# Kernel tuning notes

Measured on AMD Instinct MI355X. Metric: run time of the kernel, lower is better.

The kernel has to match this reference:

```python
import jax, jax.numpy as jnp
import numpy as np
import math

V = 4096; E = 768; H = 12; NL = 4; FFN = 2048; B = 1; L = 2048; HD = E // H
EPS = 1e-5

def _alibi_slopes(n):
    def pow2(m):
        start = 2.0 ** (-2.0 ** (-(math.log2(m) - 3)))
        return [start * start ** i for i in range(m)]
    if math.log2(n).is_integer():
        return np.array(pow2(n), dtype=np.float32)
    c = 2 ** math.floor(math.log2(n))
    s = pow2(c) + pow2(2 * c)[0::2][: n - c]
    return np.array(s, dtype=np.float32)

def _alibi_bias():
    slopes = _alibi_slopes(H)                                   # (H,)
    pos = np.arange(L)
    rel = (pos[None, :] - pos[:, None]).astype(np.float32)      # (L,L), j - i
    return jnp.asarray(slopes[:, None, None] * rel[None])       # (H,L,L)

def _ln(x, g, b):
    m = x.mean(-1, keepdims=True)
    v = ((x - m) ** 2).mean(-1, keepdims=True)
    return (x - m) / jnp.sqrt(v + EPS) * g + b

def setup_inputs():
    key = jax.random.key(0)
    ks = jax.random.split(key, 10)
    s = 0.02
    def rn(k, shape):
        return jax.random.normal(k, shape, dtype=jnp.float32) * s
    embed = rn(ks[0], (V, E)).at[0].set(0.0)   # padding_idx=0 row zeroed
    return dict(
        tokens=jax.random.randint(ks[1], (B, L), 0, V, dtype=jnp.int32),
        attention_mask=jnp.ones((B, L), dtype=jnp.int32),
        embed=embed,
        norm1_g=jnp.ones((NL, E)), norm1_b=jnp.zeros((NL, E)),
        in_w=rn(ks[2], (NL, 3 * E, E)), in_b=jnp.zeros((NL, 3 * E)),
        out_w=rn(ks[3], (NL, E, E)), out_b=jnp.zeros((NL, E)),
        ffn_g=jnp.ones((NL, E)), ffn_bt=jnp.zeros((NL, E)),
        ffn_w1=rn(ks[4], (NL, 2 * FFN, E)), ffn_b1=jnp.zeros((NL, 2 * FFN)),
        ffn_w2=rn(ks[5], (NL, E, FFN)), ffn_b2=jnp.zeros((NL, E)),
        fin_g=jnp.ones((E,)), fin_b=jnp.zeros((E,)),
        mlm_w1=rn(ks[6], (E, E)), mlm_b1=jnp.zeros((E,)),
        mlm_g=jnp.ones((E,)), mlm_bt=jnp.zeros((E,)),
        mlm_w2=rn(ks[7], (V, E)), mlm_b2=jnp.zeros((V,)),
    )

def reference(tokens, attention_mask, embed, norm1_g, norm1_b, in_w, in_b, out_w, out_b,
              ffn_g, ffn_bt, ffn_w1, ffn_b1, ffn_w2, ffn_b2,
              fin_g, fin_b, mlm_w1, mlm_b1, mlm_g, mlm_bt, mlm_w2, mlm_b2):
    x = embed[tokens]                                   # (B,L,E)
    # source adds (attention_mask == 0).float() as a FLOAT key_padding_mask
    # (torch MHA adds float masks directly to scores) -- reproduced faithfully
    key_pad = (attention_mask == 0).astype(x.dtype)     # (B,L)
    bias = _alibi_bias()[None] + key_pad[:, None, None, :]  # (B,H,L,L)
    scale = 1.0 / math.sqrt(HD)
    for i in range(NL):
        # pre-LN multi-head attention with ALiBi bias
        h = _ln(x, norm1_g[i], norm1_b[i])
        qkv = h @ in_w[i].T + in_b[i]                   # (B,L,3E)
        q, k, v = jnp.split(qkv, 3, axis=-1)
        q = q.reshape(B, L, H, HD).transpose(0, 2, 1, 3) * scale
        k = k.reshape(B, L, H, HD).transpose(0, 2, 1, 3)
        v = v.reshape(B, L, H, HD).transpose(0, 2, 1, 3)
        attn = jax.nn.softmax(jnp.einsum('bhqd,bhkd->bhqk', q, k) + bias, axis=-1)
        o = jnp.einsum('bhqk,bhkd->bhqd', attn, v).transpose(0, 2, 1, 3).reshape(B, L, E)
        x = x + (o @ out_w[i].T + out_b[i])
        # GEGLU feed-forward (pre-LN)
        h = _ln(x, ffn_g[i], ffn_bt[i])
        u = h @ ffn_w1[i].T + ffn_b1[i]                 # (B,L,2*FFN)
        a, g = jnp.split(u, 2, axis=-1)
        x = x + ((a * jax.nn.gelu(g, approximate=False)) @ ffn_w2[i].T + ffn_b2[i])
    x = _ln(x, fin_g, fin_b)
    h = jax.nn.gelu(x @ mlm_w1.T + mlm_b1, approximate=False)
    h = _ln(h, mlm_g, mlm_bt)
    return h @ mlm_w2.T + mlm_b2                        # (B,L,V) logits
```

## Files before the change

kernel.cpp:

```cpp
#include <hip/hip_runtime.h>
#include <math.h>
#include <cstdint>

#define L 2048
#define E 768
#define NH 12
#define NL 4
#define FFN 2048
#define VOC 4096
#define LDQKV (3*E)
#define LOG2E 1.4426950408889634f

typedef unsigned short u16;
typedef __bf16 bf16x8 __attribute__((ext_vector_type(8)));
typedef float f32x4 __attribute__((ext_vector_type(4)));

__device__ __forceinline__ float bf2f(u16 u){
  union { unsigned int i; float f; } v; v.i = ((unsigned int)u) << 16; return v.f;
}
__device__ __forceinline__ u16 f2bf(float f){
  union { float fl; unsigned int i; } v; v.fl = f;
  unsigned int r = v.i + 0x7fffu + ((v.i >> 16) & 1u);
  return (u16)(r >> 16);
}
__device__ __forceinline__ float gelu_exact(float x){
  return 0.5f * x * (1.0f + erff(x * 0.70710678118654752f));
}
__device__ __forceinline__ float ldw(const void* p, size_t i, int f32w){
  return f32w ? ((const float*)p)[i] : bf2f(((const u16*)p)[i]);
}

#define MFMA_BF16(a,b,c) __builtin_amdgcn_mfma_f32_16x16x32_bf16(a,b,c,0,0,0)

__device__ __forceinline__ void gload16(const u16* g, const u16* l){
  __builtin_amdgcn_global_load_lds(
      (__attribute__((address_space(1))) void*)(uintptr_t)(const void*)g,
      (__attribute__((address_space(3))) void*)(unsigned int)(uintptr_t)(const void*)l,
      16, 0, 0);
}

__global__ __launch_bounds__(256) void detect_kernel(const u16* __restrict__ emb,
                                                     unsigned int* __restrict__ flag){
  __shared__ int s;
  if (threadIdx.x == 0) s = 0;
  __syncthreads();
  float mx = 0.f;
  for (int i = threadIdx.x; i < 16384; i += 256)
    mx = fmaxf(mx, fabsf(bf2f(emb[2*i])));
  if (mx > 1e4f) s = 1;
  __syncthreads();
  if (threadIdx.x == 0) *flag = (unsigned int)s;
}

__global__ __launch_bounds__(256) void cast4_kernel(const void* __restrict__ src,
                                                    u16* __restrict__ dst, int n4,
                                                    const unsigned int* __restrict__ flag){
  int i4 = blockIdx.x * 256 + threadIdx.x;
  if (i4 >= n4) return;
  size_t i = (size_t)i4 * 4;
  ushort4 o;
  if (*flag){
    const float4 f = ((const float4*)src)[i4];
    o.x = f2bf(f.x); o.y = f2bf(f.y); o.z = f2bf(f.z); o.w = f2bf(f.w);
  } else {
    o = ((const ushort4*)src)[i4];
  }
  *(ushort4*)(dst + i) = o;
}

__global__ __launch_bounds__(256) void bias_kernel(const int* __restrict__ amask,
                                                   float* __restrict__ biasH){
  int i = blockIdx.x * 256 + threadIdx.x;
  int h = i >> 11;
  int k = i & (L - 1);
  float slope = exp2f(h < 8 ? -(float)(h+1) : -0.5f - (float)(h-8));
  float pad = (amask[k] == 0) ? 1.0f : 0.0f;
  biasH[i] = (slope * (float)k + pad) * LOG2E;
}

__global__ __launch_bounds__(256) void embed_kernel(const int* __restrict__ tok,
                                                    const void* __restrict__ emb,
                                                    const unsigned int* __restrict__ flag,
                                                    float* __restrict__ x){
  const int f32w = (int)*flag;
  int idx = blockIdx.x * 256 + threadIdx.x;
  int l = idx / E, e = idx - l * E;
  x[idx] = ldw(emb, (size_t)tok[l] * E + e, f32w);
}

__global__ __launch_bounds__(256) void ln_kernel(const float* __restrict__ x,
                                                 const void* __restrict__ g,
                                                 const void* __restrict__ b,
                                                 size_t goff, size_t boff,
                                                 const unsigned int* __restrict__ flag,
                                                 u16* __restrict__ o){
  const int f32w = (int)*flag;
  const int wave = threadIdx.x >> 6, lane = threadIdx.x & 63;
  const int row = blockIdx.x * 4 + wave;
  const float* xr = x + (size_t)row * E;
  float v[12]; float s = 0.f;
  #pragma unroll
  for (int i = 0; i < 12; i++){ v[i] = xr[lane + i*64]; s += v[i]; }
  #pragma unroll
  for (int off = 32; off > 0; off >>= 1) s += __shfl_xor(s, off);
  const float mean = s * (1.0f / E);
  float vs = 0.f;
  #pragma unroll
  for (int i = 0; i < 12; i++){ float d = v[i] - mean; vs += d * d; }
  #pragma unroll
  for (int off = 32; off > 0; off >>= 1) vs += __shfl_xor(vs, off);
  const float rstd = rsqrtf(vs * (1.0f / E) + 1e-5f);
  u16* orow = o + (size_t)row * E;
  #pragma unroll
  for (int i = 0; i < 12; i++){
    int c = lane + i*64;
    orow[c] = f2bf((v[i] - mean) * rstd * ldw(g, goff + c, f32w) + ldw(b, boff + c, f32w));
  }
}

template<int EPI>
__global__ __launch_bounds__(256)
void gemm_bt(const u16* __restrict__ A, const u16* __restrict__ Bm,
             const void* __restrict__ bias, size_t biasoff,
             const unsigned int* __restrict__ flag,
             u16* __restrict__ outb, float* __restrict__ outf,
             int M, int N, int K){
  __shared__ __align__(16) u16 As[2*128*32];
  __shared__ __align__(16) u16 Bs[2*128*32];
  const int t = threadIdx.x;
  const int lane = t & 63;
  const int col = lane & 15, quad = lane >> 4;
  const int wave = t >> 6;
  const int wr = (wave >> 1) * 64, wc = (wave & 1) * 64;
  const int row0 = blockIdx.y * 128, col0 = blockIdx.x * 128;
  const int f32w = (int)*flag;

  int kb = 0, ke = K;
  if (gridDim.z > 1){ const int kc = K / (int)gridDim.z; kb = blockIdx.z * kc; ke = kb + kc; }

  const int sr = t >> 2;
  const int sc = (t & 3) * 8;
  const u16* Ag = A + (size_t)(row0 + sr) * K + sc;
  const u16* Bg = Bm + (size_t)(col0 + sr) * K + sc;

  f32x4 acc[4][4];
  #pragma unroll
  for (int i = 0; i < 4; i++)
    #pragma unroll
    for (int j = 0; j < 4; j++) acc[i][j] = (f32x4){0.f,0.f,0.f,0.f};

  gload16(Ag + kb,                As + wave*512);
  gload16(Ag + (size_t)64*K + kb, As + wave*512 + 2048);
  gload16(Bg + kb,                Bs + wave*512);
  gload16(Bg + (size_t)64*K + kb, Bs + wave*512 + 2048);

  int p = 0;
  for (int k0 = kb; k0 < ke; k0 += 32, p ^= 1){
    if (k0 + 32 < ke){
      const int nx = (p ^ 1) * 4096;
      gload16(Ag + k0 + 32,                As + nx + wave*512);
      gload16(Ag + (size_t)64*K + k0 + 32, As + nx + wave*512 + 2048);
      gload16(Bg + k0 + 32,                Bs + nx + wave*512);
      gload16(Bg + (size_t)64*K + k0 + 32, Bs + nx + wave*512 + 2048);
      asm volatile("s_waitcnt vmcnt(4)\n\ts_barrier" ::: "memory");
    } else {
      asm volatile("s_waitcnt vmcnt(0)\n\ts_barrier" ::: "memory");
    }
    const u16* Ab = As + p*4096;
    const u16* Bb = Bs + p*4096;
    bf16x8 af[4], bfr[4];
    #pragma unroll
    for (int i = 0; i < 4; i++)
      af[i] = *(const bf16x8*)(Ab + (wr + i*16 + col)*32 + quad*8);
    #pragma unroll
    for (int j = 0; j < 4; j++)
      bfr[j] = *(const bf16x8*)(Bb + (wc + j*16 + col)*32 + quad*8);
    #pragma unroll
    for (int i = 0; i < 4; i++)
      #pragma unroll
      for (int j = 0; j < 4; j++)
        acc[i][j] = MFMA_BF16(af[i], bfr[j], acc[i][j]);
    asm volatile("s_waitcnt lgkmcnt(0)\n\ts_barrier" ::: "memory");
  }

  #pragma unroll
  for (int j = 0; j < 4; j++){
    const int c = col0 + wc + j*16 + col;
    const float bb = (gridDim.z > 1 && blockIdx.z != 0) ? 0.f : ldw(bias, biasoff + c, f32w);
    #pragma unroll
    for (int i = 0; i < 4; i++){
      const int r0 = row0 + wr + i*16 + quad*4;
      #pragma unroll
      for (int rr = 0; rr < 4; rr++){
        const float v = acc[i][j][rr] + bb;
        const size_t idx = (size_t)(r0 + rr) * N + c;
        if (EPI == 0)      outb[idx] = f2bf(v);
        else if (EPI == 1) atomicAdd(&outf[idx], v);
        else if (EPI == 2) outf[idx] = gelu_exact(v);
        else if (EPI == 3) outb[idx] = f2bf(bf2f(outb[idx]) * gelu_exact(v));
        else { if (f32w) outf[idx] = v; else outb[idx] = f2bf(v); }
      }
    }
  }
}

__global__ __launch_bounds__(256)
void vt_kernel(const u16* __restrict__ qkv, u16* __restrict__ Vt){
  const int h = blockIdx.x;
  const int t = threadIdx.x;
  const int d = t & 63;
  const int j0 = blockIdx.y * 32 + (t >> 6) * 8;
  u16 tmp[8];
  #pragma unroll
  for (int jj = 0; jj < 8; jj++)
    tmp[jj] = qkv[(size_t)(j0 + jj) * LDQKV + 2*E + h*64 + d];
  *(ushort4*)(Vt + (size_t)(h*64 + d) * L + j0)     = *(ushort4*)(tmp);
  *(ushort4*)(Vt + (size_t)(h*64 + d) * L + j0 + 4) = *(ushort4*)(tmp + 4);
}

__global__ __launch_bounds__(512, 4)
void attn_mfma(const u16* __restrict__ qkv, const u16* __restrict__ Vt,
               const float* __restrict__ biasH, u16* __restrict__ outp){
  const int head = blockIdx.x;
  const int t = threadIdx.x;
  const int wave = t >> 6, lane = t & 63;
  const int grp = wave >> 2, w4 = wave & 3;
  const int col = lane & 15, quad = lane >> 4;
  const int q0 = blockIdx.y * 64 + w4 * 16;
  const int kbeg = grp * (L/2);

  __shared__ __align__(16) u16 Kf[2][64*64];
  __shared__ __align__(16) u16 Vf[2][64*64];
  __shared__ __align__(16) u16 Pf[8][16*64];
  u16* Kg_ = Kf[grp];
  u16* Vg_ = Vf[grp];
  u16* P = Pf[wave];

  const float scale2 = 0.125f * LOG2E;
  const float* bH = biasH + (size_t)head * L + kbeg;

  const u16* qrow = qkv + (size_t)(q0 + col) * LDQKV + head*64;
  const bf16x8 qf0 = *(const bf16x8*)(qrow + quad*8);
  const bf16x8 qf1 = *(const bf16x8*)(qrow + 32 + quad*8);

  const u16* kbase  = qkv + E + head*64;
  const u16* vtbase = Vt + (size_t)(head*64) * L;

  const int tg = t & 255;
  const int skey = tg >> 2;
  const int stc  = (tg & 3) * 16;
  const int kw0  = (((skey >> 4)*8 + (tg & 3)*2)*16 + (skey & 15))*8;
  const int kw1  = kw0 + 128;

  float m_i = -1e30f, l_i = 0.f;
  f32x4 oacc[4];
  #pragma unroll
  for (int nt = 0; nt < 4; nt++) oacc[nt] = (f32x4){0.f,0.f,0.f,0.f};

  const u16* kg = kbase + (size_t)(kbeg + skey) * LDQKV + stc;
  const u16* vg = vtbase + (size_t)skey * L + kbeg + stc;
  bf16x8 kr0 = *(const bf16x8*)(kg), kr1 = *(const bf16x8*)(kg + 8);
  bf16x8 vr0 = *(const bf16x8*)(vg), vr1 = *(const bf16x8*)(vg + 8);

  for (int kt = 0; kt < L/2; kt += 64){
    *(bf16x8*)(Kg_ + kw0) = kr0;
    *(bf16x8*)(Kg_ + kw1) = kr1;
    *(bf16x8*)(Vg_ + kw0) = vr0;
    *(bf16x8*)(Vg_ + kw1) = vr1;
    asm volatile("s_waitcnt lgkmcnt(0)\n\ts_barrier" ::: "memory");
    if (kt + 64 < L/2){
      const u16* kg2 = kbase + (size_t)(kbeg + kt + 64 + skey) * LDQKV + stc;
      const u16* vg2 = vtbase + (size_t)skey * L + kbeg + kt + 64 + stc;
      kr0 = *(const bf16x8*)(kg2); kr1 = *(const bf16x8*)(kg2 + 8);
      vr0 = *(const bf16x8*)(vg2); vr1 = *(const bf16x8*)(vg2 + 8);
    }

    f32x4 s[4];
    #pragma unroll
    for (int nt = 0; nt < 4; nt++){
      const bf16x8 kf0 = *(const bf16x8*)(Kg_ + nt*1024 + lane*8);
      const bf16x8 kf1 = *(const bf16x8*)(Kg_ + nt*1024 + 512 + lane*8);
      f32x4 z = (f32x4){0.f,0.f,0.f,0.f};
      z = MFMA_BF16(kf0, qf0, z);
      z = MFMA_BF16(kf1, qf1, z);
      s[nt] = z;
    }
    float sv[16];
    #pragma unroll
    for (int nt = 0; nt < 4; nt++){
      const float4 bv = *(const float4*)(bH + kt + nt*16 + quad*4);
      sv[nt*4+0] = fmaf(s[nt][0], scale2, bv.x);
      sv[nt*4+1] = fmaf(s[nt][1], scale2, bv.y);
      sv[nt*4+2] = fmaf(s[nt][2], scale2, bv.z);
      sv[nt*4+3] = fmaf(s[nt][3], scale2, bv.w);
    }
    float t8[8];
    #pragma unroll
    for (int i = 0; i < 8; i++) t8[i] = fmaxf(sv[i], sv[i+8]);
    float t4a = fmaxf(t8[0], t8[4]), t4b = fmaxf(t8[1], t8[5]);
    float t4c = fmaxf(t8[2], t8[6]), t4d = fmaxf(t8[3], t8[7]);
    float mx = fmaxf(fmaxf(t4a, t4b), fmaxf(t4c, t4d));
    mx = fmaxf(mx, __shfl_xor(mx, 16));
    mx = fmaxf(mx, __shfl_xor(mx, 32));
    const float mnew = fmaxf(m_i, mx);
    const float a = exp2f(m_i - mnew);
    m_i = mnew;
    float ps = 0.f;
    #pragma unroll
    for (int nt = 0; nt < 4; nt++){
      const float e0 = exp2f(sv[nt*4+0] - mnew);
      const float e1 = exp2f(sv[nt*4+1] - mnew);
      const float e2 = exp2f(sv[nt*4+2] - mnew);
      const float e3 = exp2f(sv[nt*4+3] - mnew);
      unsigned int plo, phi;
      asm("v_cvt_pk_bf16_f32 %0, %1, %2" : "=v"(plo) : "v"(e0), "v"(e1));
      asm("v_cvt_pk_bf16_f32 %0, %1, %2" : "=v"(phi) : "v"(e2), "v"(e3));
      *(uint2*)(P + ((nt*2 + (quad >> 1))*16 + col)*8 + (quad & 1)*4) =
          make_uint2(plo, phi);
      ps += (e0 + e1) + (e2 + e3);
    }
    ps += __shfl_xor(ps, 16);
    ps += __shfl_xor(ps, 32);
    l_i = l_i * a + ps;
    float al[4];
    #pragma unroll
    for (int r = 0; r < 4; r++) al[r] = __shfl(a, quad*4 + r);
    #pragma unroll
    for (int nt = 0; nt < 4; nt++)
      #pragma unroll
      for (int r = 0; r < 4; r++) oacc[nt][r] *= al[r];

    asm volatile("s_waitcnt lgkmcnt(0)" ::: "memory");
    const bf16x8 pa0 = *(const bf16x8*)(P + lane*8);
    const bf16x8 pa1 = *(const bf16x8*)(P + 512 + lane*8);
    #pragma unroll
    for (int nt = 0; nt < 4; nt++){
      const bf16x8 vb0 = *(const bf16x8*)(Vg_ + nt*1024 + lane*8);
      const bf16x8 vb1 = *(const bf16x8*)(Vg_ + nt*1024 + 512 + lane*8);
      oacc[nt] = MFMA_BF16(pa0, vb0, oacc[nt]);
      oacc[nt] = MFMA_BF16(pa1, vb1, oacc[nt]);
    }
    asm volatile("s_waitcnt lgkmcnt(0)\n\ts_barrier" ::: "memory");
  }

  float* cO = (float*)&Kf[0][0];
  float* cm = (float*)&Vf[0][0];
  float* cl = cm + 64;
  if (grp == 1){
    #pragma unroll
    for (int nt = 0; nt < 4; nt++)
      #pragma unroll
      for (int r = 0; r < 4; r++)
        cO[(size_t)(w4*64 + lane)*16 + nt*4 + r] = oacc[nt][r];
    if (quad == 0){ cm[w4*16 + col] = m_i; cl[w4*16 + col] = l_i; }
  }
  __syncthreads();
  if (grp == 0){
    const float m1 = cm[w4*16 + col], l1 = cl[w4*16 + col];
    const float M = fmaxf(m_i, m1);
    const float c0 = exp2f(m_i - M), c1 = exp2f(m1 - M);
    const float inv = 1.0f / (l_i * c0 + l1 * c1);
    const float w0 = c0 * inv, w1 = c1 * inv;
    float s0[4], s1[4];
    #pragma unroll
    for (int r = 0; r < 4; r++){
      s0[r] = __shfl(w0, quad*4 + r);
      s1[r] = __shfl(w1, quad*4 + r);
    }
    #pragma unroll
    for (int nt = 0; nt < 4; nt++)
      #pragma unroll
      for (int r = 0; r < 4; r++){
        const float o1 = cO[(size_t)(w4*64 + lane)*16 + nt*4 + r];
        const int row = q0 + quad*4 + r;
        outp[(size_t)row * E + head*64 + nt*16 + col] =
            f2bf(oacc[nt][r] * s0[r] + o1 * s1[r]);
      }
  }
}

extern "C" void kernel_launch(void* const* d_in, const int* in_sizes, int n_in,
                              void* d_out, int out_size, void* d_ws, size_t ws_size,
                              hipStream_t stream){
  const int* tokens = (const int*)d_in[0];
  const int* amask  = (const int*)d_in[1];

  unsigned int* flag = (unsigned int*)d_ws;
  float* biasH = (float*)((char*)d_ws + 256);
  float* x   = biasH + (size_t)NH*L;
  u16* hbuf  = (u16*)(x + (size_t)L*E);
  u16* vtb   = hbuf + (size_t)L*E;
  u16* wc    = vtb + (size_t)NH*64*L;

  const size_t N_INW  = (size_t)NL*3*E*E;
  const size_t N_OUTW = (size_t)NL*E*E;
  const size_t N_FW1  = (size_t)NL*2*FFN*E;
  const size_t N_FW2  = (size_t)NL*E*FFN;
  const size_t N_MW1  = (size_t)E*E;
  const size_t N_MW2  = (size_t)VOC*E;
  u16* in_w  = wc;                 wc += N_INW;
  u16* out_w = wc;                 wc += N_OUTW;
  u16* ffw1  = wc;                 wc += N_FW1;
  u16* ffw2  = wc;                 wc += N_FW2;
  u16* mw1   = wc;                 wc += N_MW1;
  u16* mw2   = wc;                 wc += N_MW2;

  u16* qkvb  = (u16*)d_out;
  u16* attnb = (u16*)d_out + (size_t)L*LDQKV;
  u16* abuf  = (u16*)d_out;
  float* tbuf = (float*)d_out;

  detect_kernel<<<1, 256, 0, stream>>>((const u16*)d_in[2], flag);
  bias_kernel<<<NH*L/256, 256, 0, stream>>>(amask, biasH);
  cast4_kernel<<<(int)(N_INW/1024), 256, 0, stream>>>(d_in[5],  in_w,  (int)(N_INW/4),  flag);
  cast4_kernel<<<(int)(N_OUTW/1024),256, 0, stream>>>(d_in[7],  out_w, (int)(N_OUTW/4), flag);
  cast4_kernel<<<(int)(N_FW1/1024), 256, 0, stream>>>(d_in[11], ffw1,  (int)(N_FW1/4),  flag);
  cast4_kernel<<<(int)(N_FW2/1024), 256, 0, stream>>>(d_in[13], ffw2,  (int)(N_FW2/4),  flag);
  cast4_kernel<<<(int)(N_MW1/1024), 256, 0, stream>>>(d_in[17], mw1,   (int)(N_MW1/4),  flag);
  cast4_kernel<<<(int)(N_MW2/1024), 256, 0, stream>>>(d_in[21], mw2,   (int)(N_MW2/4),  flag);

  embed_kernel<<<L*E/256, 256, 0, stream>>>(tokens, d_in[2], flag, x);

  for (int ly = 0; ly < NL; ly++){
    ln_kernel<<<L/4, 256, 0, stream>>>(x, d_in[3], d_in[4],
        (size_t)ly*E, (size_t)ly*E, flag, hbuf);
    gemm_bt<0><<<dim3(3*E/128, L/128), 256, 0, stream>>>(hbuf, in_w + (size_t)ly*3*E*E,
        d_in[6], (size_t)ly*3*E, flag, qkvb, nullptr, L, 3*E, E);
    vt_kernel<<<dim3(NH, L/32), 256, 0, stream>>>(qkvb, vtb);
    attn_mfma<<<dim3(NH, L/64), 512, 0, stream>>>(qkvb, vtb, biasH, attnb);
    gemm_bt<1><<<dim3(E/128, L/128, 2), 256, 0, stream>>>(attnb, out_w + (size_t)ly*E*E,
        d_in[8], (size_t)ly*E, flag, nullptr, x, L, E, E);
    ln_kernel<<<L/4, 256, 0, stream>>>(x, d_in[9], d_in[10],
        (size_t)ly*E, (size_t)ly*E, flag, hbuf);
    gemm_bt<0><<<dim3(FFN/128, L/128), 256, 0, stream>>>(hbuf,
        ffw1 + (size_t)ly*2*FFN*E, d_in[12], (size_t)ly*2*FFN, flag,
        abuf, nullptr, L, FFN, E);
    gemm_bt<3><<<dim3(FFN/128, L/128), 256, 0, stream>>>(hbuf,
        ffw1 + (size_t)ly*2*FFN*E + (size_t)FFN*E, d_in[12], (size_t)ly*2*FFN + FFN, flag,
        abuf, nullptr, L, FFN, E);
    gemm_bt<1><<<dim3(E/128, L/128, 2), 256, 0, stream>>>(abuf, ffw2 + (size_t)ly*E*FFN,
        d_in[14], (size_t)ly*E, flag, nullptr, x, L, E, FFN);
  }
  ln_kernel<<<L/4, 256, 0, stream>>>(x, d_in[15], d_in[16], 0, 0, flag, hbuf);
  gemm_bt<2><<<dim3(E/128, L/128), 256, 0, stream>>>(hbuf, mw1,
      d_in[18], 0, flag, nullptr, tbuf, L, E, E);
  ln_kernel<<<L/4, 256, 0, stream>>>(tbuf, d_in[19], d_in[20], 0, 0, flag, hbuf);
  gemm_bt<4><<<dim3(VOC/128, L/128), 256, 0, stream>>>(hbuf, mw2,
      d_in[22], 0, flag, (u16*)d_out, (float*)d_out, L, VOC, E);
}
```

Before: 1.002 ms.

## Shrink GEMM tiles, restructure attention blocks with async K/V loads, fuse weight casts

GEMM tiles go from 128x128 to 64x128 so more blocks are launched to fill the many compute units. The attention kernel changes from 512-thread to 256-thread blocks that each cover 32 queries, with a swizzled block-to-head mapping and direct global-to-LDS async loads of K and V. The six weight-cast launches are merged into one kernel, and the V-transpose store is widened. The cost is less data reuse per GEMM block and more complex waitcnt/barrier sequencing in attention, which could introduce races if the counts are wrong.

```diff
diff --git a/kernel.cpp b/kernel.cpp
--- a/kernel.cpp
+++ b/kernel.cpp
@@ -52,20 +52,30 @@
   if (threadIdx.x == 0) *flag = (unsigned int)s;
 }
 
-__global__ __launch_bounds__(256) void cast4_kernel(const void* __restrict__ src,
-                                                    u16* __restrict__ dst, int n4,
-                                                    const unsigned int* __restrict__ flag){
+__global__ __launch_bounds__(256)
+void cast_all(const void* __restrict__ s0, const void* __restrict__ s1,
+              const void* __restrict__ s2, const void* __restrict__ s3,
+              const void* __restrict__ s4, const void* __restrict__ s5,
+              u16* __restrict__ dst,
+              int o1, int o2, int o3, int o4, int o5, int o6,
+              const unsigned int* __restrict__ flag){
   int i4 = blockIdx.x * 256 + threadIdx.x;
-  if (i4 >= n4) return;
-  size_t i = (size_t)i4 * 4;
+  if (i4 >= o6) return;
+  const void* src; int base;
+  if      (i4 < o1){ src = s0; base = 0;  }
+  else if (i4 < o2){ src = s1; base = o1; }
+  else if (i4 < o3){ src = s2; base = o2; }
+  else if (i4 < o4){ src = s3; base = o3; }
+  else if (i4 < o5){ src = s4; base = o4; }
+  else             { src = s5; base = o5; }
   ushort4 o;
   if (*flag){
-    const float4 f = ((const float4*)src)[i4];
+    const float4 f = ((const float4*)src)[i4 - base];
     o.x = f2bf(f.x); o.y = f2bf(f.y); o.z = f2bf(f.z); o.w = f2bf(f.w);
   } else {
-    o = ((const ushort4*)src)[i4];
-  }
-  *(ushort4*)(dst + i) = o;
+    o = ((const ushort4*)src)[i4 - base];
+  }
+  *(ushort4*)(dst + (size_t)i4 * 4) = o;
 }
 
 __global__ __launch_bounds__(256) void bias_kernel(const int* __restrict__ amask,
@@ -125,14 +135,14 @@
              const unsigned int* __restrict__ flag,
              u16* __restrict__ outb, float* __restrict__ outf,
              int M, int N, int K){
-  __shared__ __align__(16) u16 As[2*128*32];
+  __shared__ __align__(16) u16 As[2*64*32];
   __shared__ __align__(16) u16 Bs[2*128*32];
   const int t = threadIdx.x;
   const int lane = t & 63;
   const int col = lane & 15, quad = lane >> 4;
   const int wave = t >> 6;
-  const int wr = (wave >> 1) * 64, wc = (wave & 1) * 64;
-  const int row0 = blockIdx.y * 128, col0 = blockIdx.x * 128;
+  const int wr = (wave >> 1) * 32, wc = (wave & 1) * 64;
+  const int row0 = blockIdx.y * 64, col0 = blockIdx.x * 128;
   const int f32w = (int)*flag;
 
   int kb = 0, ke = K;
@@ -143,40 +153,38 @@
   const u16* Ag = A + (size_t)(row0 + sr) * K + sc;
   const u16* Bg = Bm + (size_t)(col0 + sr) * K + sc;
 
-  f32x4 acc[4][4];
-  #pragma unroll
-  for (int i = 0; i < 4; i++)
+  f32x4 acc[2][4];
+  #pragma unroll
+  for (int i = 0; i < 2; i++)
     #pragma unroll
     for (int j = 0; j < 4; j++) acc[i][j] = (f32x4){0.f,0.f,0.f,0.f};
 
   gload16(Ag + kb,                As + wave*512);
-  gload16(Ag + (size_t)64*K + kb, As + wave*512 + 2048);
   gload16(Bg + kb,                Bs + wave*512);
   gload16(Bg + (size_t)64*K + kb, Bs + wave*512 + 2048);
 
   int p = 0;
   for (int k0 = kb; k0 < ke; k0 += 32, p ^= 1){
     if (k0 + 32 < ke){
-      const int nx = (p ^ 1) * 4096;
-      gload16(Ag + k0 + 32,                As + nx + wave*512);
-      gload16(Ag + (size_t)64*K + k0 + 32, As + nx + wave*512 + 2048);
-      gload16(Bg + k0 + 32,                Bs + nx + wave*512);
-      gload16(Bg + (size_t)64*K + k0 + 32, Bs + nx + wave*512 + 2048);
-      asm volatile("s_waitcnt vmcnt(4)\n\ts_barrier" ::: "memory");
+      const int nxa = (p ^ 1) * 2048, nxb = (p ^ 1) * 4096;
+      gload16(Ag + k0 + 32,                As + nxa + wave*512);
+      gload16(Bg + k0 + 32,                Bs + nxb + wave*512);
+      gload16(Bg + (size_t)64*K + k0 + 32, Bs + nxb + wave*512 + 2048);
+      asm volatile("s_waitcnt vmcnt(3)\n\ts_barrier" ::: "memory");
     } else {
       asm volatile("s_waitcnt vmcnt(0)\n\ts_barrier" ::: "memory");
     }
-    const u16* Ab = As + p*4096;
+    const u16* Ab = As + p*2048;
     const u16* Bb = Bs + p*4096;
-    bf16x8 af[4], bfr[4];
-    #pragma unroll
-    for (int i = 0; i < 4; i++)
+    bf16x8 af[2], bfr[4];
+    #pragma unroll
+    for (int i = 0; i < 2; i++)
       af[i] = *(const bf16x8*)(Ab + (wr + i*16 + col)*32 + quad*8);
     #pragma unroll
     for (int j = 0; j < 4; j++)
       bfr[j] = *(const bf16x8*)(Bb + (wc + j*16 + col)*32 + quad*8);
     #pragma unroll
-    for (int i = 0; i < 4; i++)
+    for (int i = 0; i < 2; i++)
       #pragma unroll
       for (int j = 0; j < 4; j++)
         acc[i][j] = MFMA_BF16(af[i], bfr[j], acc[i][j]);
@@ -188,7 +196,7 @@
     const int c = col0 + wc + j*16 + col;
     const float bb = (gridDim.z > 1 && blockIdx.z != 0) ? 0.f : ldw(bias, biasoff + c, f32w);
     #pragma unroll
-    for (int i = 0; i < 4; i++){
+    for (int i = 0; i < 2; i++){
       const int r0 = row0 + wr + i*16 + quad*4;
       #pragma unroll
       for (int rr = 0; rr < 4; rr++){
@@ -210,28 +218,30 @@
   const int t = threadIdx.x;
   const int d = t & 63;
   const int j0 = blockIdx.y * 32 + (t >> 6) * 8;
-  u16 tmp[8];
+  __align__(16) u16 tmp[8];
   #pragma unroll
   for (int jj = 0; jj < 8; jj++)
     tmp[jj] = qkv[(size_t)(j0 + jj) * LDQKV + 2*E + h*64 + d];
-  *(ushort4*)(Vt + (size_t)(h*64 + d) * L + j0)     = *(ushort4*)(tmp);
-  *(ushort4*)(Vt + (size_t)(h*64 + d) * L + j0 + 4) = *(ushort4*)(tmp + 4);
-}
-
-__global__ __launch_bounds__(512, 4)
+  *(uint4*)(Vt + (size_t)(h*64 + d) * L + j0) = *(const uint4*)(tmp);
+}
+
+__global__ __launch_bounds__(256, 3)
 void attn_mfma(const u16* __restrict__ qkv, const u16* __restrict__ Vt,
                const float* __restrict__ biasH, u16* __restrict__ outp){
-  const int head = blockIdx.x;
+  const int bid = blockIdx.x;
+  const int tidx = (bid & 7) * 96 + (bid >> 3);
+  const int head = tidx >> 6;
+  const int yt = tidx & 63;
   const int t = threadIdx.x;
   const int wave = t >> 6, lane = t & 63;
-  const int grp = wave >> 2, w4 = wave & 3;
+  const int grp = wave >> 1, w2 = wave & 1;
   const int col = lane & 15, quad = lane >> 4;
-  const int q0 = blockIdx.y * 64 + w4 * 16;
+  const int q0 = yt * 32 + w2 * 16;
   const int kbeg = grp * (L/2);
 
   __shared__ __align__(16) u16 Kf[2][64*64];
   __shared__ __align__(16) u16 Vf[2][64*64];
-  __shared__ __align__(16) u16 Pf[8][16*64];
+  __shared__ __align__(16) u16 Pf[4][16*64];
   u16* Kg_ = Kf[grp];
   u16* Vg_ = Vf[grp];
   u16* P = Pf[wave];
@@ -246,34 +256,26 @@
   const u16* kbase  = qkv + E + head*64;
   const u16* vtbase = Vt + (size_t)(head*64) * L;
 
-  const int tg = t & 255;
-  const int skey = tg >> 2;
-  const int stc  = (tg & 3) * 16;
-  const int kw0  = (((skey >> 4)*8 + (tg & 3)*2)*16 + (skey & 15))*8;
-  const int kw1  = kw0 + 128;
+  const int dof = (w2*4 + quad) * 8;
+  const u16* kG = kbase  + (size_t)(kbeg + col) * LDQKV + dof;
+  const u16* vG = vtbase + (size_t)col * L + kbeg + dof;
+
+#define ISSUE_K(kt_) { _Pragma("unroll") for (int i = 0; i < 4; i++) \
+    gload16(kG + (size_t)((kt_) + i*16) * LDQKV, Kg_ + i*1024 + w2*512); }
+#define ISSUE_V(kt_) { _Pragma("unroll") for (int i = 0; i < 4; i++) \
+    gload16(vG + (size_t)(i*16) * L + (kt_), Vg_ + i*1024 + w2*512); }
 
   float m_i = -1e30f, l_i = 0.f;
   f32x4 oacc[4];
   #pragma unroll
   for (int nt = 0; nt < 4; nt++) oacc[nt] = (f32x4){0.f,0.f,0.f,0.f};
 
-  const u16* kg = kbase + (size_t)(kbeg + skey) * LDQKV + stc;
-  const u16* vg = vtbase + (size_t)skey * L + kbeg + stc;
-  bf16x8 kr0 = *(const bf16x8*)(kg), kr1 = *(const bf16x8*)(kg + 8);
-  bf16x8 vr0 = *(const bf16x8*)(vg), vr1 = *(const bf16x8*)(vg + 8);
+  ISSUE_K(0);
+  ISSUE_V(0);
 
   for (int kt = 0; kt < L/2; kt += 64){
-    *(bf16x8*)(Kg_ + kw0) = kr0;
-    *(bf16x8*)(Kg_ + kw1) = kr1;
-    *(bf16x8*)(Vg_ + kw0) = vr0;
-    *(bf16x8*)(Vg_ + kw1) = vr1;
-    asm volatile("s_waitcnt lgkmcnt(0)\n\ts_barrier" ::: "memory");
-    if (kt + 64 < L/2){
-      const u16* kg2 = kbase + (size_t)(kbeg + kt + 64 + skey) * LDQKV + stc;
-      const u16* vg2 = vtbase + (size_t)skey * L + kbeg + kt + 64 + stc;
-      kr0 = *(const bf16x8*)(kg2); kr1 = *(const bf16x8*)(kg2 + 8);
-      vr0 = *(const bf16x8*)(vg2); vr1 = *(const bf16x8*)(vg2 + 8);
-    }
+    const bool more = (kt + 64 < L/2);
+    asm volatile("s_waitcnt vmcnt(4)\n\ts_barrier" ::: "memory");
 
     f32x4 s[4];
     #pragma unroll
@@ -285,6 +287,9 @@
       z = MFMA_BF16(kf1, qf1, z);
       s[nt] = z;
     }
+    asm volatile("s_waitcnt lgkmcnt(0)\n\ts_barrier" ::: "memory");
+    if (more) ISSUE_K(kt + 64);
+
     float sv[16];
     #pragma unroll
     for (int nt = 0; nt < 4; nt++){
@@ -330,7 +335,9 @@
       #pragma unroll
       for (int r = 0; r < 4; r++) oacc[nt][r] *= al[r];
 
-    asm volatile("s_waitcnt lgkmcnt(0)" ::: "memory");
+    if (more) asm volatile("s_waitcnt vmcnt(4) lgkmcnt(0)\n\ts_barrier" ::: "memory");
+    else      asm volatile("s_waitcnt vmcnt(0) lgkmcnt(0)\n\ts_barrier" ::: "memory");
+
     const bf16x8 pa0 = *(const bf16x8*)(P + lane*8);
     const bf16x8 pa1 = *(const bf16x8*)(P + 512 + lane*8);
     #pragma unroll
@@ -341,22 +348,25 @@
       oacc[nt] = MFMA_BF16(pa1, vb1, oacc[nt]);
     }
     asm volatile("s_waitcnt lgkmcnt(0)\n\ts_barrier" ::: "memory");
-  }
+    if (more) ISSUE_V(kt + 64);
+  }
+#undef ISSUE_K
+#undef ISSUE_V
 
   float* cO = (float*)&Kf[0][0];
   float* cm = (float*)&Vf[0][0];
-  float* cl = cm + 64;
+  float* cl = cm + 32;
   if (grp == 1){
     #pragma unroll
     for (int nt = 0; nt < 4; nt++)
       #pragma unroll
       for (int r = 0; r < 4; r++)
-        cO[(size_t)(w4*64 + lane)*16 + nt*4 + r] = oacc[nt][r];
-    if (quad == 0){ cm[w4*16 + col] = m_i; cl[w4*16 + col] = l_i; }
+        cO[(size_t)(w2*64 + lane)*16 + nt*4 + r] = oacc[nt][r];
+    if (quad == 0){ cm[w2*16 + col] = m_i; cl[w2*16 + col] = l_i; }
   }
   __syncthreads();
   if (grp == 0){
-    const float m1 = cm[w4*16 + col], l1 = cl[w4*16 + col];
+    const float m1 = cm[w2*16 + col], l1 = cl[w2*16 + col];
     const float M = fmaxf(m_i, m1);
     const float c0 = exp2f(m_i - M), c1 = exp2f(m1 - M);
     const float inv = 1.0f / (l_i * c0 + l1 * c1);
@@ -371,7 +381,7 @@
     for (int nt = 0; nt < 4; nt++)
       #pragma unroll
       for (int r = 0; r < 4; r++){
-        const float o1 = cO[(size_t)(w4*64 + lane)*16 + nt*4 + r];
+        const float o1 = cO[(size_t)(w2*64 + lane)*16 + nt*4 + r];
         const int row = q0 + quad*4 + r;
         outp[(size_t)row * E + head*64 + nt*16 + col] =
             f2bf(oacc[nt][r] * s0[r] + o1 * s1[r]);
@@ -410,41 +420,44 @@
   u16* abuf  = (u16*)d_out;
   float* tbuf = (float*)d_out;
 
+  const int o1 = (int)(N_INW/4);
+  const int o2 = o1 + (int)(N_OUTW/4);
+  const int o3 = o2 + (int)(N_FW1/4);
+  const int o4 = o3 + (int)(N_FW2/4);
+  const int o5 = o4 + (int)(N_MW1/4);
+  const int o6 = o5 + (int)(N_MW2/4);
+
   detect_kernel<<<1, 256, 0, stream>>>((const u16*)d_in[2], flag);
   bias_kernel<<<NH*L/256, 256, 0, stream>>>(amask, biasH);
-  cast4_kernel<<<(int)(N_INW/1024), 256, 0, stream>>>(d_in[5],  in_w,  (int)(N_INW/4),  flag);
-  cast4_kernel<<<(int)(N_OUTW/1024),256, 0, stream>>>(d_in[7],  out_w, (int)(N_OUTW/4), flag);
-  cast4_kernel<<<(int)(N_FW1/1024), 256, 0, stream>>>(d_in[11], ffw1,  (int)(N_FW1/4),  flag);
-  cast4_kernel<<<(int)(N_FW2/1024), 256, 0, stream>>>(d_in[13], ffw2,  (int)(N_FW2/4),  flag);
-  cast4_kernel<<<(int)(N_MW1/1024), 256, 0, stream>>>(d_in[17], mw1,   (int)(N_MW1/4),  flag);
-  cast4_kernel<<<(int)(N_MW2/1024), 256, 0, stream>>>(d_in[21], mw2,   (int)(N_MW2/4),  flag);
+  cast_all<<<(o6 + 255)/256, 256, 0, stream>>>(d_in[5], d_in[7], d_in[11], d_in[13],
+      d_in[17], d_in[21], in_w, o1, o2, o3, o4, o5, o6, flag);
 
   embed_kernel<<<L*E/256, 256, 0, stream>>>(tokens, d_in[2], flag, x);
 
   for (int ly = 0; ly < NL; ly++){
     ln_kernel<<<L/4, 256, 0, stream>>>(x, d_in[3], d_in[4],
         (size_t)ly*E, (size_t)ly*E, flag, hbuf);
-    gemm_bt<0><<<dim3(3*E/128, L/128), 256, 0, stream>>>(hbuf, in_w + (size_t)ly*3*E*E,
+    gemm_bt<0><<<dim3(3*E/128, L/64), 256, 0, stream>>>(hbuf, in_w + (size_t)ly*3*E*E,
         d_in[6], (size_t)ly*3*E, flag, qkvb, nullptr, L, 3*E, E);
     vt_kernel<<<dim3(NH, L/32), 256, 0, stream>>>(qkvb, vtb);
-    attn_mfma<<<dim3(NH, L/64), 512, 0, stream>>>(qkvb, vtb, biasH, attnb);
-    gemm_bt<1><<<dim3(E/128, L/128, 2), 256, 0, stream>>>(attnb, out_w + (size_t)ly*E*E,
+    attn_mfma<<<dim3(NH * (L/32)), 256, 0, stream>>>(qkvb, vtb, biasH, attnb);
+    gemm_bt<1><<<dim3(E/128, L/64, 2), 256, 0, stream>>>(attnb, out_w + (size_t)ly*E*E,
         d_in[8], (size_t)ly*E, flag, nullptr, x, L, E, E);
     ln_kernel<<<L/4, 256, 0, stream>>>(x, d_in[9], d_in[10],
         (size_t)ly*E, (size_t)ly*E, flag, hbuf);
-    gemm_bt<0><<<dim3(FFN/128, L/128), 256, 0, stream>>>(hbuf,
+    gemm_bt<0><<<dim3(FFN/128, L/64), 256, 0, stream>>>(hbuf,
         ffw1 + (size_t)ly*2*FFN*E, d_in[12], (size_t)ly*2*FFN, flag,
         abuf, nullptr, L, FFN, E);
-    gemm_bt<3><<<dim3(FFN/128, L/128), 256, 0, stream>>>(hbuf,
+    gemm_bt<3><<<dim3(FFN/128, L/64), 256, 0, stream>>>(hbuf,
         ffw1 + (size_t)ly*2*FFN*E + (size_t)FFN*E, d_in[12], (size_t)ly*2*FFN + FFN, flag,
         abuf, nullptr, L, FFN, E);
-    gemm_bt<1><<<dim3(E/128, L/128, 2), 256, 0, stream>>>(abuf, ffw2 + (size_t)ly*E*FFN,
+    gemm_bt<1><<<dim3(E/128, L/64, 2), 256, 0, stream>>>(abuf, ffw2 + (size_t)ly*E*FFN,
         d_in[14], (size_t)ly*E, flag, nullptr, x, L, E, FFN);
   }
   ln_kernel<<<L/4, 256, 0, stream>>>(x, d_in[15], d_in[16], 0, 0, flag, hbuf);
-  gemm_bt<2><<<dim3(E/128, L/128), 256, 0, stream>>>(hbuf, mw1,
+  gemm_bt<2><<<dim3(E/128, L/64), 256, 0, stream>>>(hbuf, mw1,
       d_in[18], 0, flag, nullptr, tbuf, L, E, E);
   ln_kernel<<<L/4, 256, 0, stream>>>(tbuf, d_in[19], d_in[20], 0, 0, flag, hbuf);
-  gemm_bt<4><<<dim3(VOC/128, L/128), 256, 0, stream>>>(hbuf, mw2,
+  gemm_bt<4><<<dim3(VOC/128, L/64), 256, 0, stream>>>(hbuf, mw2,
       d_in[22], 0, flag, (u16*)d_out, (float*)d_out, L, VOC, E);
 }
```

Measured after the change: 954.0 us. -4.8%, faster.
